# Kernel tuning notes

Measured on AMD Instinct MI355X. Metric: run time of the kernel, lower is better.

## Reference

```python
import jax, jax.numpy as jnp
import numpy as np

B, C, D, H, W = 2, 3, 128, 192, 192
# spacing = (1, 1, 1) -> unit spacing, so jnp.gradient default is exact


def setup_inputs() -> dict:
    key = jax.random.key(0)
    # small displacements keep det(I + du) > 0 so log(det) is finite
    x = jax.random.normal(key, (B, C, D, H, W), dtype=jnp.float32) * 0.05
    return {"x": x}


def _jacobian_log_det_sq(x):
    # torch.gradient == numpy-style gradient: central differences in the
    # interior, one-sided differences at the boundaries.
    eye = jnp.eye(3, dtype=x.dtype)
    rows = []
    for j in range(3):  # derivative along spatial axis j (D, H, W)
        g = jnp.gradient(x, axis=2 + j)          # (B, C, D, H, W) = du_i/dx_j
        g = jnp.moveaxis(g, 1, -1)               # (B, D, H, W, i)
        rows.append(g + eye[j])                  # add delta_ij (identity)
    # J[..., j, i] = du_i/dx_j + delta_ij ; det is transpose-invariant
    J = jnp.stack(rows, axis=-2)                 # (B, D, H, W, 3, 3)
    det = jnp.linalg.det(J)                      # (B, D, H, W)
    return jnp.log(det) ** 2


def reference(x):
    return _jacobian_log_det_sq(x)
```

## Files before the change

### kernel.cpp

```cpp
#include <hip/hip_runtime.h>

constexpr int B = 2, C = 3, D = 128, H = 192, W = 192;
constexpr int sH = W;
constexpr int sD = H * W;
constexpr int sC = D * H * W;
constexpr int sB = C * sC;

constexpr int TH = 16;
constexpr int TW = 16;
constexpr int DC = 4;
constexpr int HX = H / TH;
constexpr int WX = (W / 4) / TW;
constexpr int NDC = D / DC;
constexpr int NB = B * NDC * HX * WX;
constexpr int ROWS = TH + 2;
constexpr int RSTR = TW + 1;
constexpr int CH_STR = ROWS * RSTR;
constexpr int BUFSZ = C * CH_STR;

__global__ __launch_bounds__(256, 4) void jac_logdet_sq(
    const float* __restrict__ x, float* __restrict__ out) {
    __shared__ float4 lds[2][BUFSZ];

    const int tid = threadIdx.x;
    const int tx = tid & 15;
    const int ty = tid >> 4;

    int bb = blockIdx.x;
    const int wx = bb % WX; bb /= WX;
    const int hx = bb % HX; bb /= HX;
    const int dch = bb % NDC;
    const int b = bb / NDC;

    const int d0 = dch * DC;
    const int h0 = hx * TH;
    const int h = h0 + ty;
    const int w0 = (wx * TW + tx) * 4;

    const float* pb = x + b * sB;
    const int cidx = h * sH + w0;

    const int hc = tid / 32;
    const int hr = (tid >> 4) & 1;
    const int htx = tid & 15;
    const int hh = hr ? ((h0 + TH < H) ? h0 + TH : H - 1)
                      : ((h0 > 0) ? h0 - 1 : 0);
    const int hidx = hh * sH + (wx * TW + htx) * 4;
    const int hlds = hc * CH_STR + (hr ? (TH + 1) : 0) * RSTR + htx;

    const float chc = (h > 0 && h < H - 1) ? 0.5f : 1.0f;

    float4 cm[3], c0[3], cp[3];

    const int dm = (d0 > 0) ? d0 - 1 : 0;
#pragma unroll
    for (int c = 0; c < 3; ++c) {
        c0[c] = *(const float4*)(pb + c * sC + d0 * sD + cidx);
        cm[c] = *(const float4*)(pb + c * sC + dm * sD + cidx);
    }
#pragma unroll
    for (int c = 0; c < 3; ++c)
        lds[0][c * CH_STR + (ty + 1) * RSTR + tx] = c0[c];
    if (tid < 96)
        lds[0][hlds] = *(const float4*)(pb + hc * sC + d0 * sD + hidx);
    __syncthreads();

    int cur = 0;
    int obase = ((b * D + d0) * H + h) * W + w0;

    for (int dd = 0; dd < DC; ++dd) {
        const int d = d0 + dd;
        const int dp = (d + 1 < D) ? d + 1 : D - 1;
        const float cdc = (d > 0 && d < D - 1) ? 0.5f : 1.0f;

#pragma unroll
        for (int c = 0; c < 3; ++c)
            cp[c] = *(const float4*)(pb + c * sC + dp * sD + cidx);
        float4 hv;
        const bool do_stage = (dd < DC - 1);
        if (do_stage && tid < 96)
            hv = *(const float4*)(pb + hc * sC + dp * sD + hidx);

        float lg[3], rg[3];
        if (tx == 0 && w0 > 0) {
#pragma unroll
            for (int c = 0; c < 3; ++c) lg[c] = pb[c * sC + d * sD + cidx - 1];
        }
        if (tx == 15 && w0 + 4 < W) {
#pragma unroll
            for (int c = 0; c < 3; ++c) rg[c] = pb[c * sC + d * sD + cidx + 4];
        }

        const float4* bufc = lds[cur];
        float gd[3][4], gh[3][4], gw[3][4];
#pragma unroll
        for (int c = 0; c < 3; ++c) {
            const float4 hp = bufc[c * CH_STR + (ty + 2) * RSTR + tx];
            const float4 hm = bufc[c * CH_STR + (ty    ) * RSTR + tx];
            gh[c][0] = (hp.x - hm.x) * chc;
            gh[c][1] = (hp.y - hm.y) * chc;
            gh[c][2] = (hp.z - hm.z) * chc;
            gh[c][3] = (hp.w - hm.w) * chc;

            gd[c][0] = (cp[c].x - cm[c].x) * cdc;
            gd[c][1] = (cp[c].y - cm[c].y) * cdc;
            gd[c][2] = (cp[c].z - cm[c].z) * cdc;
            gd[c][3] = (cp[c].w - cm[c].w) * cdc;

            const float lft = (tx == 0) ? lg[c]
                : bufc[c * CH_STR + (ty + 1) * RSTR + tx - 1].w;
            const float rgt = (tx == 15) ? rg[c]
                : bufc[c * CH_STR + (ty + 1) * RSTR + tx + 1].x;
            gw[c][0] = (w0 == 0)     ? (c0[c].y - c0[c].x)
                                     : 0.5f * (c0[c].y - lft);
            gw[c][1] = 0.5f * (c0[c].z - c0[c].x);
            gw[c][2] = 0.5f * (c0[c].w - c0[c].y);
            gw[c][3] = (w0 + 4 == W) ? (c0[c].w - c0[c].z)
                                     : 0.5f * (rgt - c0[c].z);
        }

        float r[4];
#pragma unroll
        for (int e = 0; e < 4; ++e) {
            const float a00 = gd[0][e] + 1.0f, a01 = gd[1][e], a02 = gd[2][e];
            const float a10 = gh[0][e], a11 = gh[1][e] + 1.0f, a12 = gh[2][e];
            const float a20 = gw[0][e], a21 = gw[1][e], a22 = gw[2][e] + 1.0f;
            const float det = a00 * (a11 * a22 - a12 * a21)
                            - a01 * (a10 * a22 - a12 * a20)
                            + a02 * (a10 * a21 - a11 * a20);
            const float l = __logf(det);
            r[e] = l * l;
        }
        *(float4*)(out + obase) = make_float4(r[0], r[1], r[2], r[3]);
        obase += sD;

        if (do_stage) {
            const int nxt = cur ^ 1;
#pragma unroll
            for (int c = 0; c < 3; ++c)
                lds[nxt][c * CH_STR + (ty + 1) * RSTR + tx] = cp[c];
            if (tid < 96) lds[nxt][hlds] = hv;
            __syncthreads();
            cur = nxt;
        }

#pragma unroll
        for (int c = 0; c < 3; ++c) { cm[c] = c0[c]; c0[c] = cp[c]; }
    }
}

extern "C" void kernel_launch(void* const* d_in, const int* in_sizes, int n_in,
                              void* d_out, int out_size, void* d_ws, size_t ws_size,
                              hipStream_t stream) {
    const float* x = (const float*)d_in[0];
    float* out = (float*)d_out;
    jac_logdet_sq<<<dim3(NB), dim3(256), 0, stream>>>(x, out);
}
```

Baseline: 178.3 us.

## Prefetch next depth plane into registers and double depth chunk per block

Software-pipelines the depth loop: the plane two steps ahead, the H-halo row and the W-edge scalars are loaded into registers one iteration early, so global load latency overlaps with the current plane's determinant and log work. The loop is fully unrolled so the LDS buffer index becomes a compile-time constant. The depth chunk per block grows from 4 to 8, which halves how often the cm/c0 boundary planes are re-read. In exchange, register pressure rises and there are half as many blocks, which can lower occupancy or leave an uneven tail wave.

```diff
diff --git a/kernel.cpp b/kernel.cpp
--- a/kernel.cpp
+++ b/kernel.cpp
@@ -8,7 +8,7 @@
 
 constexpr int TH = 16;
 constexpr int TW = 16;
-constexpr int DC = 4;
+constexpr int DC = 8;
 constexpr int HX = H / TH;
 constexpr int WX = (W / 4) / TW;
 constexpr int NDC = D / DC;
@@ -50,49 +50,71 @@
 
     const float chc = (h > 0 && h < H - 1) ? 0.5f : 1.0f;
 
-    float4 cm[3], c0[3], cp[3];
+    float4 cm[3], c0[3], cp[3], cn[3];
+    float4 hv0, hvp, hvn;
+    float lg[3], rg[3], lgn[3], rgn[3];
 
     const int dm = (d0 > 0) ? d0 - 1 : 0;
 #pragma unroll
     for (int c = 0; c < 3; ++c) {
         c0[c] = *(const float4*)(pb + c * sC + d0 * sD + cidx);
         cm[c] = *(const float4*)(pb + c * sC + dm * sD + cidx);
+        cp[c] = *(const float4*)(pb + c * sC + (d0 + 1) * sD + cidx);
+    }
+    if (tid < 96) {
+        hv0 = *(const float4*)(pb + hc * sC + d0 * sD + hidx);
+        hvp = *(const float4*)(pb + hc * sC + (d0 + 1) * sD + hidx);
+    }
+    if (tx == 0 && w0 > 0) {
+#pragma unroll
+        for (int c = 0; c < 3; ++c) lg[c] = pb[c * sC + d0 * sD + cidx - 1];
+    }
+    if (tx == 15 && w0 + 4 < W) {
+#pragma unroll
+        for (int c = 0; c < 3; ++c) rg[c] = pb[c * sC + d0 * sD + cidx + 4];
     }
 #pragma unroll
     for (int c = 0; c < 3; ++c)
         lds[0][c * CH_STR + (ty + 1) * RSTR + tx] = c0[c];
-    if (tid < 96)
-        lds[0][hlds] = *(const float4*)(pb + hc * sC + d0 * sD + hidx);
+    if (tid < 96) lds[0][hlds] = hv0;
     __syncthreads();
 
-    int cur = 0;
     int obase = ((b * D + d0) * H + h) * W + w0;
 
+#pragma unroll
     for (int dd = 0; dd < DC; ++dd) {
         const int d = d0 + dd;
-        const int dp = (d + 1 < D) ? d + 1 : D - 1;
         const float cdc = (d > 0 && d < D - 1) ? 0.5f : 1.0f;
+        const float4* bufc = lds[dd & 1];
 
+        float gd[3][4], gh[3][4], gw[3][4];
 #pragma unroll
-        for (int c = 0; c < 3; ++c)
-            cp[c] = *(const float4*)(pb + c * sC + dp * sD + cidx);
-        float4 hv;
-        const bool do_stage = (dd < DC - 1);
-        if (do_stage && tid < 96)
-            hv = *(const float4*)(pb + hc * sC + dp * sD + hidx);
-
-        float lg[3], rg[3];
-        if (tx == 0 && w0 > 0) {
-#pragma unroll
-            for (int c = 0; c < 3; ++c) lg[c] = pb[c * sC + d * sD + cidx - 1];
-        }
-        if (tx == 15 && w0 + 4 < W) {
-#pragma unroll
-            for (int c = 0; c < 3; ++c) rg[c] = pb[c * sC + d * sD + cidx + 4];
+        for (int c = 0; c < 3; ++c) {
+            gd[c][0] = (cp[c].x - cm[c].x) * cdc;
+            gd[c][1] = (cp[c].y - cm[c].y) * cdc;
+            gd[c][2] = (cp[c].z - cm[c].z) * cdc;
+            gd[c][3] = (cp[c].w - cm[c].w) * cdc;
         }
 
-        const float4* bufc = lds[cur];
-        float gd[3][4], gh[3][4], gw[3][4];
+        if (dd < DC - 1) {
+            const int dpp = (d + 2 < D) ? d + 2 : D - 1;
+#pragma unroll
+            for (int c = 0; c < 3; ++c)
+                cn[c] = *(const float4*)(pb + c * sC + dpp * sD + cidx);
+            if (dd < DC - 2 && tid < 96)
+                hvn = *(const float4*)(pb + hc * sC + dpp * sD + hidx);
+            if (tx == 0 && w0 > 0) {
+#pragma unroll
+                for (int c = 0; c < 3; ++c)
+                    lgn[c] = pb[c * sC + (d + 1) * sD + cidx - 1];
+            }
+            if (tx == 15 && w0 + 4 < W) {
+#pragma unroll
+                for (int c = 0; c < 3; ++c)
+                    rgn[c] = pb[c * sC + (d + 1) * sD + cidx + 4];
+            }
+        }
+
 #pragma unroll
         for (int c = 0; c < 3; ++c) {
             const float4 hp = bufc[c * CH_STR + (ty + 2) * RSTR + tx];
@@ -101,11 +123,6 @@
             gh[c][1] = (hp.y - hm.y) * chc;
             gh[c][2] = (hp.z - hm.z) * chc;
             gh[c][3] = (hp.w - hm.w) * chc;
-
-            gd[c][0] = (cp[c].x - cm[c].x) * cdc;
-            gd[c][1] = (cp[c].y - cm[c].y) * cdc;
-            gd[c][2] = (cp[c].z - cm[c].z) * cdc;
-            gd[c][3] = (cp[c].w - cm[c].w) * cdc;
 
             const float lft = (tx == 0) ? lg[c]
                 : bufc[c * CH_STR + (ty + 1) * RSTR + tx - 1].w;
@@ -134,18 +151,20 @@
         *(float4*)(out + obase) = make_float4(r[0], r[1], r[2], r[3]);
         obase += sD;
 
-        if (do_stage) {
-            const int nxt = cur ^ 1;
+        if (dd < DC - 1) {
 #pragma unroll
             for (int c = 0; c < 3; ++c)
-                lds[nxt][c * CH_STR + (ty + 1) * RSTR + tx] = cp[c];
-            if (tid < 96) lds[nxt][hlds] = hv;
+                lds[(dd + 1) & 1][c * CH_STR + (ty + 1) * RSTR + tx] = cp[c];
+            if (tid < 96) lds[(dd + 1) & 1][hlds] = hvp;
             __syncthreads();
-            cur = nxt;
-        }
 
 #pragma unroll
-        for (int c = 0; c < 3; ++c) { cm[c] = c0[c]; c0[c] = cp[c]; }
+            for (int c = 0; c < 3; ++c) {
+                cm[c] = c0[c]; c0[c] = cp[c]; cp[c] = cn[c];
+                lg[c] = lgn[c]; rg[c] = rgn[c];
+            }
+            hvp = hvn;
+        }
     }
 }
 
```

After: 178.4 us. Within noise of the previous version (+0.1%).
